# Performance work log

Hardware: AMD Instinct MI355X
Metric: run time of the kernel (lower is better)

The kernel has to match this reference:

```python
import jax, jax.numpy as jnp
import numpy as np

NA = 100000   # author nodes
NP = 100000   # paper nodes
E = 500000    # edges per relation
H = 128       # hidden size
FA = 256      # author input features
FP = 128      # paper input features
LA = 4        # author labels
LP = 7        # paper labels


def setup_inputs() -> dict:
    key = jax.random.key(0)
    ks = iter(jax.random.split(key, 48))
    def rn(shape, scale=0.05):
        return jax.random.normal(next(ks), shape, jnp.float32) * scale
    inp = {}
    inp['x_author'] = jax.random.normal(next(ks), (NA, FA), jnp.float32)
    inp['x_paper'] = jax.random.normal(next(ks), (NP, FP), jnp.float32)
    inp['edge_index_p2a'] = jax.random.randint(next(ks), (2, E), 0, 100000, jnp.int64)  # row0: paper src, row1: author dst
    inp['edge_index_a2p'] = jax.random.randint(next(ks), (2, E), 0, 100000, jnp.int64)  # row0: author src, row1: paper dst
    # layer 1 convs (per message type): lin_src, lin_dst, lin_update(2H->H)
    inp['w1_p2a_src'] = rn((FP, H)); inp['b1_p2a_src'] = rn((H,))
    inp['w1_p2a_dst'] = rn((FA, H)); inp['b1_p2a_dst'] = rn((H,))
    inp['w1_p2a_upd'] = rn((2 * H, H)); inp['b1_p2a_upd'] = rn((H,))
    inp['w1_a2p_src'] = rn((FA, H)); inp['b1_a2p_src'] = rn((H,))
    inp['w1_a2p_dst'] = rn((FP, H)); inp['b1_a2p_dst'] = rn((H,))
    inp['w1_a2p_upd'] = rn((2 * H, H)); inp['b1_a2p_upd'] = rn((H,))
    # layer 2 convs (all dims = H)
    inp['w2_p2a_src'] = rn((H, H)); inp['b2_p2a_src'] = rn((H,))
    inp['w2_p2a_dst'] = rn((H, H)); inp['b2_p2a_dst'] = rn((H,))
    inp['w2_p2a_upd'] = rn((2 * H, H)); inp['b2_p2a_upd'] = rn((H,))
    inp['w2_a2p_src'] = rn((H, H)); inp['b2_a2p_src'] = rn((H,))
    inp['w2_a2p_dst'] = rn((H, H)); inp['b2_a2p_dst'] = rn((H,))
    inp['w2_a2p_upd'] = rn((2 * H, H)); inp['b2_a2p_upd'] = rn((H,))
    # batchnorm affine params per node type per layer
    inp['g1_a'] = jnp.ones((H,), jnp.float32); inp['be1_a'] = jnp.zeros((H,), jnp.float32)
    inp['g1_p'] = jnp.ones((H,), jnp.float32); inp['be1_p'] = jnp.zeros((H,), jnp.float32)
    inp['g2_a'] = jnp.ones((H,), jnp.float32); inp['be2_a'] = jnp.zeros((H,), jnp.float32)
    inp['g2_p'] = jnp.ones((H,), jnp.float32); inp['be2_p'] = jnp.zeros((H,), jnp.float32)
    # post message-passing heads
    inp['w_post_a'] = rn((H, LA)); inp['b_post_a'] = rn((LA,))
    inp['w_post_p'] = rn((H, LP)); inp['b_post_p'] = rn((LP,))
    return inp


def _mean_agg(x_src, src, dst, n_dst):
    # gather source features along edges, mean-scatter to destination nodes
    msg = x_src[src]                                            # [E, F]
    s = jax.ops.segment_sum(msg, dst, num_segments=n_dst)       # [n_dst, F]
    cnt = jax.ops.segment_sum(jnp.ones((dst.shape[0],), msg.dtype), dst, num_segments=n_dst)
    return s / jnp.maximum(cnt, 1.0)[:, None]


def _conv(x_src, x_dst, src, dst, ws, bs, wd, bd, wu, bu):
    agg = _mean_agg(x_src, src, dst, x_dst.shape[0])
    h = jnp.concatenate([x_dst @ wd + bd, agg @ ws + bs], axis=-1)   # [n_dst, 2H]
    return h @ wu + bu


def _bn_lrelu(x, g, b):
    # BatchNorm1d(eps=1) in training mode (batch stats, biased var) then LeakyReLU(0.01)
    m = x.mean(axis=0)
    v = x.var(axis=0)
    y = g * (x - m) / jnp.sqrt(v + 1.0) + b
    return jnp.where(y >= 0, y, 0.01 * y)


def reference(x_author, x_paper, edge_index_p2a, edge_index_a2p,
              w1_p2a_src, b1_p2a_src, w1_p2a_dst, b1_p2a_dst, w1_p2a_upd, b1_p2a_upd,
              w1_a2p_src, b1_a2p_src, w1_a2p_dst, b1_a2p_dst, w1_a2p_upd, b1_a2p_upd,
              w2_p2a_src, b2_p2a_src, w2_p2a_dst, b2_p2a_dst, w2_p2a_upd, b2_p2a_upd,
              w2_a2p_src, b2_a2p_src, w2_a2p_dst, b2_a2p_dst, w2_a2p_upd, b2_a2p_upd,
              g1_a, be1_a, g1_p, be1_p, g2_a, be2_a, g2_p, be2_p,
              w_post_a, b_post_a, w_post_p, b_post_p):
    src_pa, dst_pa = edge_index_p2a[0], edge_index_p2a[1]
    src_ap, dst_ap = edge_index_a2p[0], edge_index_a2p[1]
    # layer 1: per-message-type conv -> per-node-type BN + LeakyReLU
    h_a = _conv(x_paper, x_author, src_pa, dst_pa, w1_p2a_src, b1_p2a_src, w1_p2a_dst, b1_p2a_dst, w1_p2a_upd, b1_p2a_upd)
    h_p = _conv(x_author, x_paper, src_ap, dst_ap, w1_a2p_src, b1_a2p_src, w1_a2p_dst, b1_a2p_dst, w1_a2p_upd, b1_a2p_upd)
    h_a = _bn_lrelu(h_a, g1_a, be1_a)
    h_p = _bn_lrelu(h_p, g1_p, be1_p)
    # layer 2
    h_a2 = _conv(h_p, h_a, src_pa, dst_pa, w2_p2a_src, b2_p2a_src, w2_p2a_dst, b2_p2a_dst, w2_p2a_upd, b2_p2a_upd)
    h_p2 = _conv(h_a, h_p, src_ap, dst_ap, w2_a2p_src, b2_a2p_src, w2_a2p_dst, b2_a2p_dst, w2_a2p_upd, b2_a2p_upd)
    h_a2 = _bn_lrelu(h_a2, g2_a, be2_a)
    h_p2 = _bn_lrelu(h_p2, g2_p, be2_p)
    # post message-passing heads per node type
    out_a = h_a2 @ w_post_a + b_post_a   # [NA, LA]
    out_p = h_p2 @ w_post_p + b_post_p   # [NP, LP]
    return (out_a, out_p)
```

## Files before the change

### kernel.cpp

```cpp
#include <hip/hip_runtime.h>

#define NN 100000
#define NE 500000
#define HD 128
#define NBLK 391

typedef float f32x4v __attribute__((ext_vector_type(4)));
typedef short s16x8  __attribute__((ext_vector_type(8)));

static __device__ __forceinline__ unsigned f2bf_bits(float f){
  unsigned u = __float_as_uint(f);
  return (u + 0x7FFF + ((u >> 16) & 1)) >> 16;
}

static __device__ __forceinline__ void split8(const float* a, s16x8& hi, s16x8& lo){
  #pragma unroll
  for (int j = 0; j < 8; ++j){
    float f = a[j];
    unsigned hb = f2bf_bits(f);
    float hf = __uint_as_float(hb << 16);
    float lf = f - hf;
    hi[j] = (short)hb;
    lo[j] = (short)f2bf_bits(lf);
  }
}

__global__ void k_count(const int* __restrict__ ei_pa, const int* __restrict__ ei_ap,
                        int* __restrict__ deg2){
  int idx = blockIdx.x * 256 + threadIdx.x;
  if (idx < NE)        atomicAdd(&deg2[      ei_pa[NE + idx]], 1);
  else if (idx < 2*NE) atomicAdd(&deg2[NN + ei_ap[NE + (idx - NE)]], 1);
}

__global__ void k_bsum(const int* __restrict__ deg2, int* __restrict__ bsum){
  int rel = blockIdx.x / NBLK, b = blockIdx.x % NBLK;
  int i = b*256 + threadIdx.x;
  int v = (i < NN) ? deg2[rel*NN + i] : 0;
  __shared__ int s[256];
  s[threadIdx.x] = v; __syncthreads();
  for (int o = 128; o > 0; o >>= 1){
    if (threadIdx.x < o) s[threadIdx.x] += s[threadIdx.x + o];
    __syncthreads();
  }
  if (threadIdx.x == 0) bsum[rel*512 + b] = s[0];
}

__global__ void k_bscan(const int* __restrict__ bsum, int* __restrict__ bsoff){
  int rel = blockIdx.x, t = threadIdx.x;
  int v = (t < NBLK) ? bsum[rel*512 + t] : 0;
  __shared__ int s[512];
  s[t] = v; __syncthreads();
  for (int o = 1; o < 512; o <<= 1){
    int x = (t >= o) ? s[t - o] : 0;
    __syncthreads();
    s[t] += x;
    __syncthreads();
  }
  bsoff[rel*512 + t] = s[t] - v;
}

__global__ void k_scanC(const int* __restrict__ deg2, const int* __restrict__ bsoff,
                        int* __restrict__ off2, int* __restrict__ cur2){
  int rel = blockIdx.x / NBLK, b = blockIdx.x % NBLK;
  int i = b*256 + threadIdx.x, t = threadIdx.x;
  int v = (i < NN) ? deg2[rel*NN + i] : 0;
  __shared__ int s[256];
  s[t] = v; __syncthreads();
  for (int o = 1; o < 256; o <<= 1){
    int x = (t >= o) ? s[t - o] : 0;
    __syncthreads();
    s[t] += x;
    __syncthreads();
  }
  if (i < NN){
    int o = bsoff[rel*512 + b] + s[t] - v;
    off2[rel*NN + i] = o;
    cur2[rel*NN + i] = o;
  }
}

__global__ void k_fill(const int* __restrict__ ei_pa, const int* __restrict__ ei_ap,
                       int* __restrict__ cur2,
                       int* __restrict__ col_pa, int* __restrict__ col_ap){
  int idx = blockIdx.x * 256 + threadIdx.x;
  if (idx < NE){
    int s = ei_pa[idx], d = ei_pa[NE + idx];
    int pos = atomicAdd(&cur2[d], 1);
    col_pa[pos] = s;
  } else if (idx < 2*NE){
    int e = idx - NE;
    int s = ei_ap[e], d = ei_ap[NE + e];
    int pos = atomicAdd(&cur2[NN + d], 1);
    col_ap[pos] = s;
  }
}

struct FoldDesc { const float* A; const float* B; short* T; int off; };
struct FoldArgs { FoldDesc d[8]; int rs[9]; };

__global__ void k_fold(FoldArgs fa){
  int row = blockIdx.x;
  int seg = 0;
  #pragma unroll
  for (int s = 0; s < 8; ++s) if (row >= fa.rs[s+1]) seg = s + 1;
  int m = row - fa.rs[seg];
  const float* A = fa.d[seg].A + (size_t)m * 128;
  const float* B = fa.d[seg].B;
  int n = threadIdx.x;
  float acc = 0.f;
  for (int k = 0; k < 128; ++k) acc += A[k] * B[k*128 + n];
  unsigned hb = f2bf_bits(acc);
  float hf = __uint_as_float(hb << 16);
  unsigned lb = f2bf_bits(acc - hf);
  int gkc = fa.d[seg].off + (m >> 5), quad = (m >> 3) & 3, j = m & 7;
  int lane = quad*16 + (n & 15), nt = n >> 4;
  size_t fb = (size_t)((gkc*8 + nt)*2)*512 + lane*8 + j;
  fa.d[seg].T[fb]       = (short)hb;
  fa.d[seg].T[fb + 512] = (short)lb;
}

struct BiasArgs { const float* bd[4]; const float* bs[4]; const float* wu[4];
                  const float* bu[4]; float* outb[4]; };
__global__ void k_biasfold(BiasArgs ba){
  int s = blockIdx.x, j = threadIdx.x;
  const float* wu = ba.wu[s];
  float acc = ba.bu[s][j];
  for (int k = 0; k < 128; ++k)
    acc += ba.bd[s][k] * wu[k*128 + j] + ba.bs[s][k] * wu[(128 + k)*128 + j];
  ba.outb[s][j] = acc;
}

__global__ __launch_bounds__(256)
void k_gemm2(const float* __restrict__ A1, int lda1, int KC1,
             const float* __restrict__ A2, int lda2, int KC2,
             const short* __restrict__ Bf,
             const float* __restrict__ bias, const float* __restrict__ extra,
             float* __restrict__ C, float* __restrict__ stats, int M)
{
  __shared__ __align__(16) char smem[65536];
  short* Bs = (short*)smem;

  const int tid  = threadIdx.x;
  const int wave = tid >> 6, lane = tid & 63;
  const int li   = lane & 15, quad = lane >> 4;
  const int rowT = blockIdx.x * 128 + wave * 32;
  const int KCtot = KC1 + KC2;

  f32x4v acc[2][8];
  #pragma unroll
  for (int mt = 0; mt < 2; ++mt)
    #pragma unroll
    for (int nt = 0; nt < 8; ++nt)
      acc[mt][nt] = (f32x4v){0.f, 0.f, 0.f, 0.f};

  float4 c0[2], c1[2], n0[2], n1[2];
  auto loadA = [&](int gkc, float4* p0, float4* p1){
    const float* Ab; int ld, kk;
    if (gkc < KC1){ Ab = A1; ld = lda1; kk = gkc; }
    else          { Ab = A2; ld = lda2; kk = gkc - KC1; }
    #pragma unroll
    for (int mt = 0; mt < 2; ++mt){
      int row = rowT + mt*16 + li;
      if (row < M){
        const float* ap = Ab + (size_t)row*ld + kk*32 + quad*8;
        p0[mt] = *(const float4*)ap;
        p1[mt] = *(const float4*)(ap + 4);
      } else {
        p0[mt] = make_float4(0.f,0.f,0.f,0.f);
        p1[mt] = make_float4(0.f,0.f,0.f,0.f);
      }
    }
  };
  loadA(0, c0, c1);

  for (int g = 0; g < KCtot; g += 4){
    if (g > 0) __syncthreads();
    const short* src = Bf + (size_t)g*8192;
    #pragma unroll
    for (int c2 = 0; c2 < 16; ++c2){
      int id = c2*256 + tid;
      *(s16x8*)(Bs + id*8) = *(const s16x8*)(src + id*8);
    }
    __syncthreads();
    #pragma unroll
    for (int kc = 0; kc < 4; ++kc){
      int gkc = g + kc;
      if (gkc + 1 < KCtot) loadA(gkc + 1, n0, n1);
      s16x8 ah[2], al[2];
      #pragma unroll
      for (int mt = 0; mt < 2; ++mt){
        float av[8] = {c0[mt].x, c0[mt].y, c0[mt].z, c0[mt].w,
                       c1[mt].x, c1[mt].y, c1[mt].z, c1[mt].w};
        split8(av, ah[mt], al[mt]);
      }
      #pragma unroll
      for (int nt = 0; nt < 8; ++nt){
        const short* bp = Bs + ((kc*8 + nt) << 10) + lane*8;
        s16x8 bh = *(const s16x8*)bp;
        s16x8 bl = *(const s16x8*)(bp + 512);
        #pragma unroll
        for (int mt = 0; mt < 2; ++mt){
          acc[mt][nt] = __builtin_amdgcn_mfma_f32_16x16x32_bf16(ah[mt], bh, acc[mt][nt], 0, 0, 0);
          acc[mt][nt] = __builtin_amdgcn_mfma_f32_16x16x32_bf16(al[mt], bh, acc[mt][nt], 0, 0, 0);
          acc[mt][nt] = __builtin_amdgcn_mfma_f32_16x16x32_bf16(ah[mt], bl, acc[mt][nt], 0, 0, 0);
        }
      }
      #pragma unroll
      for (int mt = 0; mt < 2; ++mt){ c0[mt] = n0[mt]; c1[mt] = n1[mt]; }
    }
  }

  __syncthreads();
  float* Cs = (float*)smem;
  #pragma unroll
  for (int mt = 0; mt < 2; ++mt)
    #pragma unroll
    for (int r = 0; r < 4; ++r){
      int lrow = wave*32 + mt*16 + quad*4 + r;
      #pragma unroll
      for (int nt = 0; nt < 8; ++nt)
        Cs[lrow*128 + nt*16 + li] = acc[mt][nt][r];
    }
  int col4 = lane & 31;
  float4 bias4 = make_float4(0.f,0.f,0.f,0.f);
  if (bias) bias4 = ((const float4*)bias)[col4];
  float4 s1 = make_float4(0.f,0.f,0.f,0.f), s2 = s1;
  #pragma unroll
  for (int i = 0; i < 16; ++i){
    int row  = wave*32 + i*2 + (lane >> 5);
    int grow = blockIdx.x*128 + row;
    if (grow >= M) continue;
    float4 v = ((const float4*)(Cs + row*128))[col4];
    v.x += bias4.x; v.y += bias4.y; v.z += bias4.z; v.w += bias4.w;
    if (extra){
      float4 e = ((const float4*)(extra + (size_t)grow*128))[col4];
      v.x += e.x; v.y += e.y; v.z += e.z; v.w += e.w;
    }
    ((float4*)(C + (size_t)grow*128))[col4] = v;
    s1.x += v.x; s1.y += v.y; s1.z += v.z; s1.w += v.w;
    s2.x += v.x*v.x; s2.y += v.y*v.y; s2.z += v.z*v.z; s2.w += v.w*v.w;
  }
  if (stats){
    __syncthreads();
    float* Ss = (float*)smem;
    ((float4*)Ss)[tid*2]     = s1;
    ((float4*)Ss)[tid*2 + 1] = s2;
    __syncthreads();
    int c = tid & 127, kind = tid >> 7;
    int cc4 = c >> 2, comp = c & 3;
    float s = 0.f;
    #pragma unroll
    for (int wv = 0; wv < 4; ++wv)
      #pragma unroll
      for (int hf = 0; hf < 2; ++hf)
        s += Ss[(wv*64 + hf*32 + cc4)*8 + kind*4 + comp];
    atomicAdd(&stats[kind*128 + c], s);
  }
}

__global__ __launch_bounds__(256)
void k_agg(const float* __restrict__ t, const int* __restrict__ off,
           const int* __restrict__ deg, const int* __restrict__ col,
           float* __restrict__ o){
  int slot = threadIdx.x >> 5, col4 = threadIdx.x & 31;
  int d = blockIdx.x*8 + slot;
  if (d >= NN) return;
  int s0 = off[d], cnt = deg[d];
  float4 a0 = make_float4(0.f,0.f,0.f,0.f), a1 = a0;
  int i = 0;
  for (; i + 2 <= cnt; i += 2){
    int sa = col[s0 + i], sb = col[s0 + i + 1];
    float4 va = ((const float4*)(t + (size_t)sa*128))[col4];
    float4 vb = ((const float4*)(t + (size_t)sb*128))[col4];
    a0.x += va.x; a0.y += va.y; a0.z += va.z; a0.w += va.w;
    a1.x += vb.x; a1.y += vb.y; a1.z += vb.z; a1.w += vb.w;
  }
  if (i < cnt){
    int sa = col[s0 + i];
    float4 va = ((const float4*)(t + (size_t)sa*128))[col4];
    a0.x += va.x; a0.y += va.y; a0.z += va.z; a0.w += va.w;
  }
  float inv = 1.0f / (float)(cnt > 0 ? cnt : 1);
  float4 r;
  r.x = (a0.x + a1.x)*inv; r.y = (a0.y + a1.y)*inv;
  r.z = (a0.z + a1.z)*inv; r.w = (a0.w + a1.w)*inv;
  ((float4*)(o + (size_t)d*128))[col4] = r;
}

__global__ void k_bnprep(const float* __restrict__ stats, const float* __restrict__ g,
                         const float* __restrict__ b, float* __restrict__ sc, int M){
  int c = threadIdx.x;
  float invN = 1.0f / (float)M;
  float m  = stats[c] * invN;
  float var = stats[128 + c] * invN - m*m;
  float scale = g[c] / sqrtf(var + 1.0f);
  sc[c] = scale;
  sc[128 + c] = b[c] - m*scale;
}

__global__ void k_bn(float* __restrict__ x, const float* __restrict__ sc, int M){
  int idx = blockIdx.x*256 + threadIdx.x;
  if (idx >= M*32) return;
  int c = (idx & 31) * 4;
  float4 v = ((float4*)x)[idx];
  float s0=sc[c],s1=sc[c+1],s2=sc[c+2],s3=sc[c+3];
  float h0=sc[128+c],h1=sc[129+c],h2=sc[130+c],h3=sc[131+c];
  v.x = v.x*s0 + h0; v.x = v.x >= 0.f ? v.x : 0.01f*v.x;
  v.y = v.y*s1 + h1; v.y = v.y >= 0.f ? v.y : 0.01f*v.y;
  v.z = v.z*s2 + h2; v.z = v.z >= 0.f ? v.z : 0.01f*v.z;
  v.w = v.w*s3 + h3; v.w = v.w >= 0.f ? v.w : 0.01f*v.w;
  ((float4*)x)[idx] = v;
}

template<int LC>
__global__ void k_head(const float* __restrict__ h, const float* __restrict__ w,
                       const float* __restrict__ b, float* __restrict__ o, int M){
  __shared__ float ws[128*LC];
  __shared__ float bs[LC];
  for (int i = threadIdx.x; i < 128*LC; i += 256) ws[i] = w[i];
  if (threadIdx.x < LC) bs[threadIdx.x] = b[threadIdx.x];
  __syncthreads();
  int r = blockIdx.x*256 + threadIdx.x;
  if (r >= M) return;
  float acc[LC];
  #pragma unroll
  for (int c = 0; c < LC; ++c) acc[c] = bs[c];
  const float4* hr = (const float4*)(h + (size_t)r*128);
  for (int k4 = 0; k4 < 32; ++k4){
    float4 v = hr[k4];
    int k = k4*4;
    #pragma unroll
    for (int c = 0; c < LC; ++c)
      acc[c] += v.x*ws[k*LC+c] + v.y*ws[(k+1)*LC+c] + v.z*ws[(k+2)*LC+c] + v.w*ws[(k+3)*LC+c];
  }
  #pragma unroll
  for (int c = 0; c < LC; ++c) o[(size_t)r*LC + c] = acc[c];
}

extern "C" void kernel_launch(void* const* d_in, const int* in_sizes, int n_in,
                              void* d_out, int out_size, void* d_ws, size_t ws_size,
                              hipStream_t stream) {
  const float* x_author = (const float*)d_in[0];
  const float* x_paper  = (const float*)d_in[1];
  const int*   ei_pa    = (const int*)d_in[2];
  const int*   ei_ap    = (const int*)d_in[3];

  char* p = (char*)d_ws;
  auto alloc = [&](size_t bytes) -> void* {
    void* r = (void*)p; p += (bytes + 255) & ~(size_t)255; return r;
  };
  short* T_l1a  = (short*)alloc(12u*16384);
  short* T_l1ps = (short*)alloc( 8u*16384);
  short* T_l1pd = (short*)alloc( 4u*16384);
  short* T_l2a  = (short*)alloc( 8u*16384);
  short* T_l2p  = (short*)alloc( 8u*16384);
  float* w1a_b = (float*)alloc(128*4);      float* w1p_b = (float*)alloc(128*4);
  float* w2a_b = (float*)alloc(128*4);      float* w2p_b = (float*)alloc(128*4);
  float* stats4 = (float*)alloc(4*256*4);
  float* bnsc  = (float*)alloc(256*4);
  int* deg2  = (int*)alloc(2*NN*4);
  int* off2  = (int*)alloc(2*NN*4);
  int* cur2  = (int*)alloc(2*NN*4);
  int* col_pa = (int*)alloc(NE*4);
  int* col_ap = (int*)alloc(NE*4);
  int* bsum  = (int*)alloc(1024*4);
  int* bsoff = (int*)alloc(1024*4);
  const size_t NB = (size_t)NN * 128;
  float* B1 = (float*)alloc(NB*4);
  float* B2 = (float*)alloc(NB*4);
  float* B3 = (float*)alloc(NB*4);
  float* B4 = (float*)alloc(NB*4);

  hipMemsetAsync(deg2, 0, 2*NN*4, stream);
  hipMemsetAsync(stats4, 0, 4*256*4, stream);
  k_count<<<(2*NE + 255)/256, 256, 0, stream>>>(ei_pa, ei_ap, deg2);
  k_bsum <<<2*NBLK, 256, 0, stream>>>(deg2, bsum);
  k_bscan<<<2, 512, 0, stream>>>(bsum, bsoff);
  k_scanC<<<2*NBLK, 256, 0, stream>>>(deg2, bsoff, off2, cur2);
  k_fill <<<(2*NE + 255)/256, 256, 0, stream>>>(ei_pa, ei_ap, cur2, col_pa, col_ap);

  FoldArgs fa;
  const float* wu1a = (const float*)d_in[8];
  const float* wu1p = (const float*)d_in[14];
  const float* wu2a = (const float*)d_in[20];
  const float* wu2p = (const float*)d_in[26];
  fa.d[0] = { (const float*)d_in[6],  wu1a,           T_l1a,  0 };
  fa.d[1] = { (const float*)d_in[4],  wu1a + 128*128, T_l1a,  8 };
  fa.d[2] = { (const float*)d_in[10], wu1p + 128*128, T_l1ps, 0 };
  fa.d[3] = { (const float*)d_in[12], wu1p,           T_l1pd, 0 };
  fa.d[4] = { (const float*)d_in[18], wu2a,           T_l2a,  0 };
  fa.d[5] = { (const float*)d_in[16], wu2a + 128*128, T_l2a,  4 };
  fa.d[6] = { (const float*)d_in[24], wu2p,           T_l2p,  0 };
  fa.d[7] = { (const float*)d_in[22], wu2p + 128*128, T_l2p,  4 };
  int rows[8] = {256,128,256,128,128,128,128,128};
  fa.rs[0] = 0;
  for (int i = 0; i < 8; ++i) fa.rs[i+1] = fa.rs[i] + rows[i];
  k_fold<<<fa.rs[8], 128, 0, stream>>>(fa);

  BiasArgs ba;
  ba.bd[0]=(const float*)d_in[7];  ba.bs[0]=(const float*)d_in[5];  ba.wu[0]=wu1a; ba.bu[0]=(const float*)d_in[9];  ba.outb[0]=w1a_b;
  ba.bd[1]=(const float*)d_in[13]; ba.bs[1]=(const float*)d_in[11]; ba.wu[1]=wu1p; ba.bu[1]=(const float*)d_in[15]; ba.outb[1]=w1p_b;
  ba.bd[2]=(const float*)d_in[19]; ba.bs[2]=(const float*)d_in[17]; ba.wu[2]=wu2a; ba.bu[2]=(const float*)d_in[21]; ba.outb[2]=w2a_b;
  ba.bd[3]=(const float*)d_in[25]; ba.bs[3]=(const float*)d_in[23]; ba.wu[3]=wu2p; ba.bu[3]=(const float*)d_in[27]; ba.outb[3]=w2p_b;
  k_biasfold<<<4, 128, 0, stream>>>(ba);

  const int GG = (NN + 127)/128;
  const int AGG_GRID = (NN + 7)/8;
  const int* off_pa = off2;        const int* deg_pa = deg2;
  const int* off_ap = off2 + NN;   const int* deg_ap = deg2 + NN;
  float* st_a1 = stats4;       float* st_p1 = stats4 + 256;
  float* st_a2 = stats4 + 512; float* st_p2 = stats4 + 768;

  k_agg<<<AGG_GRID, 256, 0, stream>>>(x_paper, off_pa, deg_pa, col_pa, B4);
  k_gemm2<<<GG, 256, 0, stream>>>(x_author, 256, 8, B4, 128, 4, T_l1a,
                                  w1a_b, nullptr, B1, st_a1, NN);
  k_bnprep<<<1, 128, 0, stream>>>(st_a1, (const float*)d_in[28], (const float*)d_in[29], bnsc, NN);
  k_bn<<<NN*32/256, 256, 0, stream>>>(B1, bnsc, NN);

  k_gemm2<<<GG, 256, 0, stream>>>(x_author, 256, 8, nullptr, 0, 0, T_l1ps,
                                  nullptr, nullptr, B3, nullptr, NN);
  k_agg<<<AGG_GRID, 256, 0, stream>>>(B3, off_ap, deg_ap, col_ap, B4);
  k_gemm2<<<GG, 256, 0, stream>>>(x_paper, 128, 4, nullptr, 0, 0, T_l1pd,
                                  w1p_b, B4, B2, st_p1, NN);
  k_bnprep<<<1, 128, 0, stream>>>(st_p1, (const float*)d_in[30], (const float*)d_in[31], bnsc, NN);
  k_bn<<<NN*32/256, 256, 0, stream>>>(B2, bnsc, NN);

  k_agg<<<AGG_GRID, 256, 0, stream>>>(B2, off_pa, deg_pa, col_pa, B4);
  k_gemm2<<<GG, 256, 0, stream>>>(B1, 128, 4, B4, 128, 4, T_l2a,
                                  w2a_b, nullptr, B3, st_a2, NN);
  k_bnprep<<<1, 128, 0, stream>>>(st_a2, (const float*)d_in[32], (const float*)d_in[33], bnsc, NN);
  k_bn<<<NN*32/256, 256, 0, stream>>>(B3, bnsc, NN);
  k_head<4><<<(NN + 255)/256, 256, 0, stream>>>(B3, (const float*)d_in[36], (const float*)d_in[37],
                                                (float*)d_out, NN);

  k_agg<<<AGG_GRID, 256, 0, stream>>>(B1, off_ap, deg_ap, col_ap, B4);
  k_gemm2<<<GG, 256, 0, stream>>>(B2, 128, 4, B4, 128, 4, T_l2p,
                                  w2p_b, nullptr, B1, st_p2, NN);
  k_bnprep<<<1, 128, 0, stream>>>(st_p2, (const float*)d_in[34], (const float*)d_in[35], bnsc, NN);
  k_bn<<<NN*32/256, 256, 0, stream>>>(B1, bnsc, NN);
  k_head<7><<<(NN + 255)/256, 256, 0, stream>>>(B1, (const float*)d_in[38], (const float*)d_in[39],
                                                (float*)d_out + (size_t)NN*4, NN);
}
```

Measured before the change: 874.4 us.

## Fuse BatchNorm+LeakyReLU into consumers, shrink GEMM LDS for occupancy, unroll aggregation

```diff
diff --git a/kernel.cpp b/kernel.cpp
--- a/kernel.cpp
+++ b/kernel.cpp
@@ -23,6 +23,14 @@
     hi[j] = (short)hb;
     lo[j] = (short)f2bf_bits(lf);
   }
+}
+
+static __device__ __forceinline__ float4 bn_lrelu4(float4 v, float4 sc, float4 sh){
+  v.x = v.x*sc.x + sh.x; v.x = v.x >= 0.f ? v.x : 0.01f*v.x;
+  v.y = v.y*sc.y + sh.y; v.y = v.y >= 0.f ? v.y : 0.01f*v.y;
+  v.z = v.z*sc.z + sh.z; v.z = v.z >= 0.f ? v.z : 0.01f*v.z;
+  v.w = v.w*sc.w + sh.w; v.w = v.w >= 0.f ? v.w : 0.01f*v.w;
+  return v;
 }
 
 __global__ void k_count(const int* __restrict__ ei_pa, const int* __restrict__ ei_ap,
@@ -130,14 +138,15 @@
   ba.outb[s][j] = acc;
 }
 
-__global__ __launch_bounds__(256)
+__global__ __launch_bounds__(256, 4)
 void k_gemm2(const float* __restrict__ A1, int lda1, int KC1,
+             const float* __restrict__ bn1,
              const float* __restrict__ A2, int lda2, int KC2,
              const short* __restrict__ Bf,
              const float* __restrict__ bias, const float* __restrict__ extra,
              float* __restrict__ C, float* __restrict__ stats, int M)
 {
-  __shared__ __align__(16) char smem[65536];
+  __shared__ __align__(16) char smem[32768];
   short* Bs = (short*)smem;
 
   const int tid  = threadIdx.x;
@@ -155,16 +164,24 @@
 
   float4 c0[2], c1[2], n0[2], n1[2];
   auto loadA = [&](int gkc, float4* p0, float4* p1){
-    const float* Ab; int ld, kk;
-    if (gkc < KC1){ Ab = A1; ld = lda1; kk = gkc; }
-    else          { Ab = A2; ld = lda2; kk = gkc - KC1; }
+    const float* Ab; int ld, kk; bool bn;
+    if (gkc < KC1){ Ab = A1; ld = lda1; kk = gkc; bn = (bn1 != nullptr); }
+    else          { Ab = A2; ld = lda2; kk = gkc - KC1; bn = false; }
+    float4 sc0, sc1, sh0, sh1;
+    if (bn){
+      const float* bsc = bn1 + kk*32 + quad*8;
+      sc0 = *(const float4*)bsc;        sc1 = *(const float4*)(bsc + 4);
+      sh0 = *(const float4*)(bsc+128);  sh1 = *(const float4*)(bsc + 132);
+    }
     #pragma unroll
     for (int mt = 0; mt < 2; ++mt){
       int row = rowT + mt*16 + li;
       if (row < M){
         const float* ap = Ab + (size_t)row*ld + kk*32 + quad*8;
-        p0[mt] = *(const float4*)ap;
-        p1[mt] = *(const float4*)(ap + 4);
+        float4 v0 = *(const float4*)ap;
+        float4 v1 = *(const float4*)(ap + 4);
+        if (bn){ v0 = bn_lrelu4(v0, sc0, sh0); v1 = bn_lrelu4(v1, sc1, sh1); }
+        p0[mt] = v0; p1[mt] = v1;
       } else {
         p0[mt] = make_float4(0.f,0.f,0.f,0.f);
         p1[mt] = make_float4(0.f,0.f,0.f,0.f);
@@ -173,17 +190,17 @@
   };
   loadA(0, c0, c1);
 
-  for (int g = 0; g < KCtot; g += 4){
+  for (int g = 0; g < KCtot; g += 2){
     if (g > 0) __syncthreads();
     const short* src = Bf + (size_t)g*8192;
     #pragma unroll
-    for (int c2 = 0; c2 < 16; ++c2){
+    for (int c2 = 0; c2 < 8; ++c2){
       int id = c2*256 + tid;
       *(s16x8*)(Bs + id*8) = *(const s16x8*)(src + id*8);
     }
     __syncthreads();
     #pragma unroll
-    for (int kc = 0; kc < 4; ++kc){
+    for (int kc = 0; kc < 2; ++kc){
       int gkc = g + kc;
       if (gkc + 1 < KCtot) loadA(gkc + 1, n0, n1);
       s16x8 ah[2], al[2];
@@ -211,34 +228,39 @@
   }
 
   __syncthreads();
-  float* Cs = (float*)smem;
-  #pragma unroll
-  for (int mt = 0; mt < 2; ++mt)
-    #pragma unroll
-    for (int r = 0; r < 4; ++r){
-      int lrow = wave*32 + mt*16 + quad*4 + r;
-      #pragma unroll
-      for (int nt = 0; nt < 8; ++nt)
-        Cs[lrow*128 + nt*16 + li] = acc[mt][nt][r];
-    }
+  float* Cw = (float*)smem + wave*2048;
   int col4 = lane & 31;
   float4 bias4 = make_float4(0.f,0.f,0.f,0.f);
   if (bias) bias4 = ((const float4*)bias)[col4];
   float4 s1 = make_float4(0.f,0.f,0.f,0.f), s2 = s1;
   #pragma unroll
-  for (int i = 0; i < 16; ++i){
-    int row  = wave*32 + i*2 + (lane >> 5);
-    int grow = blockIdx.x*128 + row;
-    if (grow >= M) continue;
-    float4 v = ((const float4*)(Cs + row*128))[col4];
-    v.x += bias4.x; v.y += bias4.y; v.z += bias4.z; v.w += bias4.w;
-    if (extra){
-      float4 e = ((const float4*)(extra + (size_t)grow*128))[col4];
-      v.x += e.x; v.y += e.y; v.z += e.z; v.w += e.w;
-    }
-    ((float4*)(C + (size_t)grow*128))[col4] = v;
-    s1.x += v.x; s1.y += v.y; s1.z += v.z; s1.w += v.w;
-    s2.x += v.x*v.x; s2.y += v.y*v.y; s2.z += v.z*v.z; s2.w += v.w*v.w;
+  for (int mt = 0; mt < 2; ++mt){
+    #pragma unroll
+    for (int r = 0; r < 4; ++r){
+      int lr = quad*4 + r;
+      #pragma unroll
+      for (int nt = 0; nt < 8; ++nt){
+        int c = nt*16 + li;
+        int chunk = ((c >> 2) + 2*quad) & 31;
+        Cw[lr*128 + chunk*4 + (c & 3)] = acc[mt][nt][r];
+      }
+    }
+    #pragma unroll
+    for (int i = 0; i < 8; ++i){
+      int lr = i*2 + (lane >> 5);
+      int grow = rowT + mt*16 + lr;
+      if (grow >= M) continue;
+      int chunk = (col4 + 2*(lr >> 2)) & 31;
+      float4 v = *(const float4*)(Cw + lr*128 + chunk*4);
+      v.x += bias4.x; v.y += bias4.y; v.z += bias4.z; v.w += bias4.w;
+      if (extra){
+        float4 e = ((const float4*)(extra + (size_t)grow*128))[col4];
+        v.x += e.x; v.y += e.y; v.z += e.z; v.w += e.w;
+      }
+      ((float4*)(C + (size_t)grow*128))[col4] = v;
+      s1.x += v.x; s1.y += v.y; s1.z += v.z; s1.w += v.w;
+      s2.x += v.x*v.x; s2.y += v.y*v.y; s2.z += v.z*v.z; s2.w += v.w*v.w;
+    }
   }
   if (stats){
     __syncthreads();
@@ -261,24 +283,34 @@
 __global__ __launch_bounds__(256)
 void k_agg(const float* __restrict__ t, const int* __restrict__ off,
            const int* __restrict__ deg, const int* __restrict__ col,
-           float* __restrict__ o){
+           float* __restrict__ o, const float* __restrict__ bn){
   int slot = threadIdx.x >> 5, col4 = threadIdx.x & 31;
   int d = blockIdx.x*8 + slot;
   if (d >= NN) return;
+  float4 sc4, sh4;
+  bool hasbn = (bn != nullptr);
+  if (hasbn){ sc4 = ((const float4*)bn)[col4]; sh4 = ((const float4*)(bn+128))[col4]; }
   int s0 = off[d], cnt = deg[d];
   float4 a0 = make_float4(0.f,0.f,0.f,0.f), a1 = a0;
   int i = 0;
-  for (; i + 2 <= cnt; i += 2){
-    int sa = col[s0 + i], sb = col[s0 + i + 1];
-    float4 va = ((const float4*)(t + (size_t)sa*128))[col4];
-    float4 vb = ((const float4*)(t + (size_t)sb*128))[col4];
-    a0.x += va.x; a0.y += va.y; a0.z += va.z; a0.w += va.w;
-    a1.x += vb.x; a1.y += vb.y; a1.z += vb.z; a1.w += vb.w;
-  }
-  if (i < cnt){
-    int sa = col[s0 + i];
-    float4 va = ((const float4*)(t + (size_t)sa*128))[col4];
-    a0.x += va.x; a0.y += va.y; a0.z += va.z; a0.w += va.w;
+  for (; i + 4 <= cnt; i += 4){
+    int sa = col[s0+i], sb = col[s0+i+1], sct = col[s0+i+2], sd = col[s0+i+3];
+    float4 v0 = ((const float4*)(t + (size_t)sa*128))[col4];
+    float4 v1 = ((const float4*)(t + (size_t)sb*128))[col4];
+    float4 v2 = ((const float4*)(t + (size_t)sct*128))[col4];
+    float4 v3 = ((const float4*)(t + (size_t)sd*128))[col4];
+    if (hasbn){
+      v0 = bn_lrelu4(v0, sc4, sh4); v1 = bn_lrelu4(v1, sc4, sh4);
+      v2 = bn_lrelu4(v2, sc4, sh4); v3 = bn_lrelu4(v3, sc4, sh4);
+    }
+    a0.x += v0.x + v2.x; a0.y += v0.y + v2.y; a0.z += v0.z + v2.z; a0.w += v0.w + v2.w;
+    a1.x += v1.x + v3.x; a1.y += v1.y + v3.y; a1.z += v1.z + v3.z; a1.w += v1.w + v3.w;
+  }
+  for (; i < cnt; ++i){
+    int sa = col[s0+i];
+    float4 v0 = ((const float4*)(t + (size_t)sa*128))[col4];
+    if (hasbn) v0 = bn_lrelu4(v0, sc4, sh4);
+    a0.x += v0.x; a0.y += v0.y; a0.z += v0.z; a0.w += v0.w;
   }
   float inv = 1.0f / (float)(cnt > 0 ? cnt : 1);
   float4 r;
@@ -298,27 +330,16 @@
   sc[128 + c] = b[c] - m*scale;
 }
 
-__global__ void k_bn(float* __restrict__ x, const float* __restrict__ sc, int M){
-  int idx = blockIdx.x*256 + threadIdx.x;
-  if (idx >= M*32) return;
-  int c = (idx & 31) * 4;
-  float4 v = ((float4*)x)[idx];
-  float s0=sc[c],s1=sc[c+1],s2=sc[c+2],s3=sc[c+3];
-  float h0=sc[128+c],h1=sc[129+c],h2=sc[130+c],h3=sc[131+c];
-  v.x = v.x*s0 + h0; v.x = v.x >= 0.f ? v.x : 0.01f*v.x;
-  v.y = v.y*s1 + h1; v.y = v.y >= 0.f ? v.y : 0.01f*v.y;
-  v.z = v.z*s2 + h2; v.z = v.z >= 0.f ? v.z : 0.01f*v.z;
-  v.w = v.w*s3 + h3; v.w = v.w >= 0.f ? v.w : 0.01f*v.w;
-  ((float4*)x)[idx] = v;
-}
-
 template<int LC>
-__global__ void k_head(const float* __restrict__ h, const float* __restrict__ w,
-                       const float* __restrict__ b, float* __restrict__ o, int M){
+__global__ void k_head(const float* __restrict__ h, const float* __restrict__ bn,
+                       const float* __restrict__ w, const float* __restrict__ b,
+                       float* __restrict__ o, int M){
   __shared__ float ws[128*LC];
   __shared__ float bs[LC];
+  __shared__ float bsc[256];
   for (int i = threadIdx.x; i < 128*LC; i += 256) ws[i] = w[i];
   if (threadIdx.x < LC) bs[threadIdx.x] = b[threadIdx.x];
+  if (threadIdx.x < 256) bsc[threadIdx.x] = bn[threadIdx.x];
   __syncthreads();
   int r = blockIdx.x*256 + threadIdx.x;
   if (r >= M) return;
@@ -328,6 +349,9 @@
   const float4* hr = (const float4*)(h + (size_t)r*128);
   for (int k4 = 0; k4 < 32; ++k4){
     float4 v = hr[k4];
+    float4 sc = ((const float4*)bsc)[k4];
+    float4 sh = ((const float4*)bsc)[32 + k4];
+    v = bn_lrelu4(v, sc, sh);
     int k = k4*4;
     #pragma unroll
     for (int c = 0; c < LC; ++c)
@@ -357,7 +381,7 @@
   float* w1a_b = (float*)alloc(128*4);      float* w1p_b = (float*)alloc(128*4);
   float* w2a_b = (float*)alloc(128*4);      float* w2p_b = (float*)alloc(128*4);
   float* stats4 = (float*)alloc(4*256*4);
-  float* bnsc  = (float*)alloc(256*4);
+  float* bnsc4  = (float*)alloc(4*256*4);
   int* deg2  = (int*)alloc(2*NN*4);
   int* off2  = (int*)alloc(2*NN*4);
   int* cur2  = (int*)alloc(2*NN*4);
@@ -410,34 +434,32 @@
   const int* off_ap = off2 + NN;   const int* deg_ap = deg2 + NN;
   float* st_a1 = stats4;       float* st_p1 = stats4 + 256;
   float* st_a2 = stats4 + 512; float* st_p2 = stats4 + 768;
-
-  k_agg<<<AGG_GRID, 256, 0, stream>>>(x_paper, off_pa, deg_pa, col_pa, B4);
-  k_gemm2<<<GG, 256, 0, stream>>>(x_author, 256, 8, B4, 128, 4, T_l1a,
+  float* sc_a1 = bnsc4;        float* sc_p1 = bnsc4 + 256;
+  float* sc_a2 = bnsc4 + 512;  float* sc_p2 = bnsc4 + 768;
+
+  k_agg<<<AGG_GRID, 256, 0, stream>>>(x_paper, off_pa, deg_pa, col_pa, B4, nullptr);
+  k_gemm2<<<GG, 256, 0, stream>>>(x_author, 256, 8, nullptr, B4, 128, 4, T_l1a,
                                   w1a_b, nullptr, B1, st_a1, NN);
-  k_bnprep<<<1, 128, 0, stream>>>(st_a1, (const float*)d_in[28], (const float*)d_in[29], bnsc, NN);
-  k_bn<<<NN*32/256, 256, 0, stream>>>(B1, bnsc, NN);
-
-  k_gemm2<<<GG, 256, 0, stream>>>(x_author, 256, 8, nullptr, 0, 0, T_l1ps,
+  k_bnprep<<<1, 128, 0, stream>>>(st_a1, (const float*)d_in[28], (const float*)d_in[29], sc_a1, NN);
+
+  k_gemm2<<<GG, 256, 0, stream>>>(x_author, 256, 8, nullptr, nullptr, 0, 0, T_l1ps,
                                   nullptr, nullptr, B3, nullptr, NN);
-  k_agg<<<AGG_GRID, 256, 0, stream>>>(B3, off_ap, deg_ap, col_ap, B4);
-  k_gemm2<<<GG, 256, 0, stream>>>(x_paper, 128, 4, nullptr, 0, 0, T_l1pd,
+  k_agg<<<AGG_GRID, 256, 0, stream>>>(B3, off_ap, deg_ap, col_ap, B4, nullptr);
+  k_gemm2<<<GG, 256, 0, stream>>>(x_paper, 128, 4, nullptr, nullptr, 0, 0, T_l1pd,
                                   w1p_b, B4, B2, st_p1, NN);
-  k_bnprep<<<1, 128, 0, stream>>>(st_p1, (const float*)d_in[30], (const float*)d_in[31], bnsc, NN);
-  k_bn<<<NN*32/256, 256, 0, stream>>>(B2, bnsc, NN);
-
-  k_agg<<<AGG_GRID, 256, 0, stream>>>(B2, off_pa, deg_pa, col_pa, B4);
-  k_gemm2<<<GG, 256, 0, stream>>>(B1, 128, 4, B4, 128, 4, T_l2a,
+  k_bnprep<<<1, 128, 0, stream>>>(st_p1, (const float*)d_in[30], (const float*)d_in[31], sc_p1, NN);
+
+  k_agg<<<AGG_GRID, 256, 0, stream>>>(B2, off_pa, deg_pa, col_pa, B4, sc_p1);
+  k_gemm2<<<GG, 256, 0, stream>>>(B1, 128, 4, sc_a1, B4, 128, 4, T_l2a,
                                   w2a_b, nullptr, B3, st_a2, NN);
-  k_bnprep<<<1, 128, 0, stream>>>(st_a2, (const float*)d_in[32], (const float*)d_in[33], bnsc, NN);
-  k_bn<<<NN*32/256, 256, 0, stream>>>(B3, bnsc, NN);
-  k_head<4><<<(NN + 255)/256, 256, 0, stream>>>(B3, (const float*)d_in[36], (const float*)d_in[37],
-                                                (float*)d_out, NN);
-
-  k_agg<<<AGG_GRID, 256, 0, stream>>>(B1, off_ap, deg_ap, col_ap, B4);
-  k_gemm2<<<GG, 256, 0, stream>>>(B2, 128, 4, B4, 128, 4, T_l2p,
-                                  w2p_b, nullptr, B1, st_p2, NN);
-  k_bnprep<<<1, 128, 0, stream>>>(st_p2, (const float*)d_in[34], (const float*)d_in[35], bnsc, NN);
-  k_bn<<<NN*32/256, 256, 0, stream>>>(B1, bnsc, NN);
-  k_head<7><<<(NN + 255)/256, 256, 0, stream>>>(B1, (const float*)d_in[38], (const float*)d_in[39],
-                                                (float*)d_out + (size_t)NN*4, NN);
-}
+  k_bnprep<<<1, 128, 0, stream>>>(st_a2, (const float*)d_in[32], (const float*)d_in[33], sc_a2, NN);
+  k_head<4><<<(NN + 255)/256, 256, 0, stream>>>(B3, sc_a2, (const float*)d_in[36],
+                                                (const float*)d_in[37], (float*)d_out, NN);
+
+  k_agg<<<AGG_GRID, 256, 0, stream>>>(B1, off_ap, deg_ap, col_ap, B4, sc_a1);
+  k_gemm2<<<GG, 256, 0, stream>>>(B2, 128, 4, sc_p1, B4, 128, 4, T_l2p,
+                                  w2p_b, nullptr, B3, st_p2, NN);
+  k_bnprep<<<1, 128, 0, stream>>>(st_p2, (const float*)d_in[34], (const float*)d_in[35], sc_p2, NN);
+  k_head<7><<<(NN + 255)/256, 256, 0, stream>>>(B3, sc_p2, (const float*)d_in[38],
+                                                (const float*)d_in[39], (float*)d_out + (size_t)NN*4, NN);
+}
```

Measured after the change: 898.8 us. 2.8% more time.
